# Kernel tuning notes

Measured on AMD Instinct MI355X. Metric: run time of the kernel, lower is better.

Reference implementation:

```python
import jax, jax.numpy as jnp
import numpy as np

N_NODES = 50000


def gcn_conv(x, W, b, src, dst, n):
    """PyG-style GCNConv: out = D^-1/2 (A+I) D^-1/2 (x W) + b.
    src/dst: [E] int edge endpoints (messages flow src -> dst)."""
    h = x @ W  # [n, out]
    # degree with self-loops (edge weight 1)
    deg = jax.ops.segment_sum(jnp.ones_like(dst, dtype=h.dtype), dst, num_segments=n) + 1.0
    inv_sqrt = jax.lax.rsqrt(deg)  # [n]
    coef = inv_sqrt[src] * inv_sqrt[dst]  # [E]
    msg = h[src] * coef[:, None]  # [E, out]
    agg = jax.ops.segment_sum(msg, dst, num_segments=n)
    # self-loop contribution: norm = 1/deg
    agg = agg + h * (inv_sqrt * inv_sqrt)[:, None]
    return agg + b


def encoder(x, src, dst, W_a, b_a, W_b, b_b, n):
    h = jax.nn.relu(gcn_conv(x, W_a, b_a, src, dst, n))
    return jax.nn.relu(gcn_conv(h, W_b, b_b, src, dst, n))


def setup_inputs() -> dict:
    key = jax.random.key(0)
    ks = jax.random.split(key, 8)
    N, E = N_NODES, 400000
    d_in, d_hid, d_out = 512, 512, 256
    x = jax.random.normal(ks[0], (N, d_in), dtype=jnp.float32)
    edge_index = jax.random.randint(ks[1], (2, E), 0, N, dtype=jnp.int32)
    edge_index2 = jax.random.randint(ks[2], (2, E), 0, N, dtype=jnp.int32)

    def xavier(k, shape):
        lim = np.sqrt(6.0 / (shape[0] + shape[1]))
        return jax.random.uniform(k, shape, jnp.float32, -lim, lim)

    W1 = xavier(ks[3], (d_in, d_hid))
    b1 = jnp.zeros((d_hid,), jnp.float32)
    W2 = xavier(ks[4], (d_hid, d_out))
    b2 = jnp.zeros((d_out,), jnp.float32)
    W3 = xavier(ks[5], (d_out, d_hid))
    b3 = jnp.zeros((d_hid,), jnp.float32)
    W4 = xavier(ks[6], (d_hid, d_out))
    b4 = jnp.zeros((d_out,), jnp.float32)
    return {"x": x, "edge_index": edge_index, "edge_index2": edge_index2,
            "W1": W1, "b1": b1, "W2": W2, "b2": b2,
            "W3": W3, "b3": b3, "W4": W4, "b4": b4}


def reference(x, edge_index, edge_index2, W1, b1, W2, b2, W3, b3, W4, b4):
    n = x.shape[0]
    z = encoder(x, edge_index[0], edge_index[1], W1, b1, W2, b2, n)
    z_g = encoder(z, edge_index2[0], edge_index2[1], W3, b3, W4, b4, n)
    return (z, z_g)
```

## Files before the change

### kernel.cpp

```cpp
#include <hip/hip_runtime.h>

#define N_NODES 50000
#define MP 50048

typedef short short8 __attribute__((ext_vector_type(8)));
typedef float floatx4 __attribute__((ext_vector_type(4)));
typedef ushort u16x4 __attribute__((ext_vector_type(4)));
typedef ushort u16x8 __attribute__((ext_vector_type(8)));
typedef float f32x4 __attribute__((ext_vector_type(4)));

__device__ __forceinline__ float bf2f(ushort u) {
    union { unsigned int i; float f; } x; x.i = ((unsigned int)u) << 16; return x.f;
}
__device__ __forceinline__ ushort f2bf(float f) {
    union { float f; unsigned int i; } x; x.f = f;
    unsigned int r = x.i + 0x7FFFu + ((x.i >> 16) & 1u);
    return (ushort)(r >> 16);
}

__global__ __launch_bounds__(256) void deg_int_kernel(const int* __restrict__ dst,
                                                      int* __restrict__ deg, int E) {
    int i = blockIdx.x * 256 + threadIdx.x;
    if (i < E) atomicAdd(&deg[dst[i]], 1);
}
__global__ __launch_bounds__(256) void inv_from_deg(const int* __restrict__ deg,
                                                    float* __restrict__ inv, int n) {
    int i = blockIdx.x * 256 + threadIdx.x;
    if (i < n) inv[i] = rsqrtf((float)deg[i] + 1.0f);
}

__global__ __launch_bounds__(256) void scan1_kernel(const int* __restrict__ deg,
                                                    int* __restrict__ pre,
                                                    int* __restrict__ bsum, int n) {
    __shared__ int tmp[256];
    const int t = threadIdx.x;
    const int i = blockIdx.x * 256 + t;
    const int v = (i < n) ? deg[i] : 0;
    tmp[t] = v;
    __syncthreads();
#pragma unroll
    for (int d = 1; d < 256; d <<= 1) {
        int u = (t >= d) ? tmp[t - d] : 0;
        __syncthreads();
        tmp[t] += u;
        __syncthreads();
    }
    if (i < n) pre[i] = tmp[t] - v;
    if (t == 255) bsum[blockIdx.x] = tmp[255];
}
__global__ __launch_bounds__(256) void scan2_kernel(int* __restrict__ bsum, int nb,
                                                    int* __restrict__ row_ptr_n) {
    __shared__ int tmp[256];
    const int t = threadIdx.x;
    const int v = (t < nb) ? bsum[t] : 0;
    tmp[t] = v;
    __syncthreads();
#pragma unroll
    for (int d = 1; d < 256; d <<= 1) {
        int u = (t >= d) ? tmp[t - d] : 0;
        __syncthreads();
        tmp[t] += u;
        __syncthreads();
    }
    if (t < nb) bsum[t] = tmp[t] - v;
    if (t == 255) *row_ptr_n = tmp[255];
}
__global__ __launch_bounds__(256) void scan3_kernel(const int* __restrict__ pre,
                                                    const int* __restrict__ bsum,
                                                    int* __restrict__ row_ptr,
                                                    int* __restrict__ cursor, int n) {
    const int i = blockIdx.x * 256 + threadIdx.x;
    if (i < n) {
        int v = pre[i] + bsum[blockIdx.x];
        row_ptr[i] = v;
        cursor[i] = v;
    }
}
__global__ __launch_bounds__(256) void fill_adj_kernel(const int* __restrict__ src,
                                                       const int* __restrict__ dst,
                                                       const float* __restrict__ invs,
                                                       int* __restrict__ cursor,
                                                       int2* __restrict__ adjw, int E) {
    int i = blockIdx.x * 256 + threadIdx.x;
    if (i < E) {
        int s = src[i];
        int pos = atomicAdd(&cursor[dst[i]], 1);
        adjw[pos] = make_int2(s, __float_as_int(invs[s]));
    }
}

__global__ __launch_bounds__(256) void transpose_kernel(const float* __restrict__ W,
                                                        ushort* __restrict__ Wt, int K, int N) {
    int idx = blockIdx.x * 256 + threadIdx.x;
    if (idx < K * N) {
        int k = idx / N, n = idx % N;
        Wt[n * K + k] = f2bf(W[idx]);
    }
}

__global__ __launch_bounds__(512, 4) void gemm_kernel(
    const ushort* __restrict__ A, const ushort* __restrict__ Bt,
    ushort* __restrict__ C, const float* __restrict__ bias,
    int M, int K, int N, int do_relu)
{
    __shared__ __align__(16) ushort Alds[128 * 32];
    __shared__ __align__(16) ushort Blds[128 * 32];
    const int t = threadIdx.x;
    const int w = t >> 6, l = t & 63;
    const int m0 = blockIdx.y * 128;
    const int n0 = blockIdx.x * 128;
    const int wr = (w >> 2) * 64, wc = (w & 3) * 32;
    const int lhi = l >> 4, llo = l & 15;

    floatx4 acc[4][2] = {};

    const int srow = w * 16 + (l >> 2);
    const int scol = (l & 3) * 8;
    int gr = m0 + srow; gr = gr < M ? gr : M - 1;
    const ushort* gA = A + (size_t)gr * K + scol;
    const ushort* gB = Bt + (size_t)(n0 + srow) * K + scol;
    ushort* lA = Alds + srow * 32 + scol;
    ushort* lB = Blds + srow * 32 + scol;

    const int nkt = K >> 5;
    for (int kt = 0; kt < nkt; ++kt) {
        const int k0 = kt << 5;
        __builtin_amdgcn_global_load_lds(
            (const __attribute__((address_space(1))) void*)(gA + k0),
            (__attribute__((address_space(3))) void*)lA, 16, 0, 0);
        __builtin_amdgcn_global_load_lds(
            (const __attribute__((address_space(1))) void*)(gB + k0),
            (__attribute__((address_space(3))) void*)lB, 16, 0, 0);
        __syncthreads();
        short8 av[4], bv[2];
#pragma unroll
        for (int m = 0; m < 4; ++m)
            av[m] = *reinterpret_cast<const short8*>(&Alds[(wr + m * 16 + llo) * 32 + lhi * 8]);
#pragma unroll
        for (int n = 0; n < 2; ++n)
            bv[n] = *reinterpret_cast<const short8*>(&Blds[(wc + n * 16 + llo) * 32 + lhi * 8]);
#pragma unroll
        for (int m = 0; m < 4; ++m)
#pragma unroll
            for (int n = 0; n < 2; ++n)
                acc[m][n] = __builtin_amdgcn_mfma_f32_16x16x32_bf16(av[m], bv[n], acc[m][n], 0, 0, 0);
        __syncthreads();
    }

    const int lr = lhi * 4;
#pragma unroll
    for (int m = 0; m < 4; ++m) {
#pragma unroll
        for (int n = 0; n < 2; ++n) {
            int gcol = n0 + wc + n * 16 + llo;
            float badd = bias ? bias[gcol] : 0.0f;
#pragma unroll
            for (int j = 0; j < 4; ++j) {
                int grow = m0 + wr + m * 16 + lr + j;
                if (grow < M) {
                    float v = acc[m][n][j] + badd;
                    if (do_relu) v = fmaxf(v, 0.0f);
                    C[(size_t)grow * N + gcol] = f2bf(v);
                }
            }
        }
    }
}

__global__ __launch_bounds__(512, 4) void gemm_f32a_kernel(
    const float* __restrict__ A, const ushort* __restrict__ Bt,
    ushort* __restrict__ C, int M, int K, int N)
{
    __shared__ __align__(16) ushort Alds[128 * 32];
    __shared__ __align__(16) ushort Blds[128 * 32];
    const int t = threadIdx.x;
    const int w = t >> 6, l = t & 63;
    const int m0 = blockIdx.y * 128;
    const int n0 = blockIdx.x * 128;
    const int wr = (w >> 2) * 64, wc = (w & 3) * 32;
    const int lhi = l >> 4, llo = l & 15;

    floatx4 acc[4][2] = {};

    const int srow = w * 16 + (l >> 2);
    const int scol = (l & 3) * 8;
    int gr = m0 + srow; gr = gr < M ? gr : M - 1;
    const float*  gA = A + (size_t)gr * K + scol;
    const ushort* gB = Bt + (size_t)(n0 + srow) * K + scol;
    ushort* lA = Alds + srow * 32 + scol;
    ushort* lB = Blds + srow * 32 + scol;

    const int nkt = K >> 5;
    for (int kt = 0; kt < nkt; ++kt) {
        const int k0 = kt << 5;
        __builtin_amdgcn_global_load_lds(
            (const __attribute__((address_space(1))) void*)(gB + k0),
            (__attribute__((address_space(3))) void*)lB, 16, 0, 0);
        const f32x4 alo = *reinterpret_cast<const f32x4*>(gA + k0);
        const f32x4 ahi = *reinterpret_cast<const f32x4*>(gA + k0 + 4);
        u16x8 ab;
#pragma unroll
        for (int k = 0; k < 4; ++k) { ab[k] = f2bf(alo[k]); ab[k + 4] = f2bf(ahi[k]); }
        *reinterpret_cast<u16x8*>(lA) = ab;
        __syncthreads();
        short8 av[4], bv[2];
#pragma unroll
        for (int m = 0; m < 4; ++m)
            av[m] = *reinterpret_cast<const short8*>(&Alds[(wr + m * 16 + llo) * 32 + lhi * 8]);
#pragma unroll
        for (int n = 0; n < 2; ++n)
            bv[n] = *reinterpret_cast<const short8*>(&Blds[(wc + n * 16 + llo) * 32 + lhi * 8]);
#pragma unroll
        for (int m = 0; m < 4; ++m)
#pragma unroll
            for (int n = 0; n < 2; ++n)
                acc[m][n] = __builtin_amdgcn_mfma_f32_16x16x32_bf16(av[m], bv[n], acc[m][n], 0, 0, 0);
        __syncthreads();
    }

    const int lr = lhi * 4;
#pragma unroll
    for (int m = 0; m < 4; ++m) {
#pragma unroll
        for (int n = 0; n < 2; ++n) {
            int gcol = n0 + wc + n * 16 + llo;
#pragma unroll
            for (int j = 0; j < 4; ++j) {
                int grow = m0 + wr + m * 16 + lr + j;
                if (grow < M)
                    C[(size_t)grow * N + gcol] = f2bf(acc[m][n][j]);
            }
        }
    }
}

__global__ __launch_bounds__(256) void gather512_kernel(
    const int* __restrict__ row_ptr, const int2* __restrict__ adjw,
    const ushort* __restrict__ h, const float* __restrict__ invs,
    const float* __restrict__ bias, ushort* __restrict__ outB)
{
    const int wv = threadIdx.x >> 6, l = threadIdx.x & 63;
    const int node = blockIdx.x * 4 + wv;
    if (node >= N_NODES) return;
    const int c0 = l * 8;
    const int beg = row_ptr[node], end = row_ptr[node + 1];
    const float invd = invs[node];

    float a0[8] = {}, a1[8] = {}, a2[8] = {}, a3[8] = {};
    int e = beg;
    for (; e + 4 <= end; e += 4) {
        const int2 w0 = adjw[e], w1 = adjw[e+1], w2 = adjw[e+2], w3 = adjw[e+3];
        const float f0 = __int_as_float(w0.y) * invd, f1 = __int_as_float(w1.y) * invd;
        const float f2 = __int_as_float(w2.y) * invd, f3 = __int_as_float(w3.y) * invd;
        const u16x8 h0 = *reinterpret_cast<const u16x8*>(h + (unsigned)(w0.x * 512 + c0));
        const u16x8 h1 = *reinterpret_cast<const u16x8*>(h + (unsigned)(w1.x * 512 + c0));
        const u16x8 h2 = *reinterpret_cast<const u16x8*>(h + (unsigned)(w2.x * 512 + c0));
        const u16x8 h3 = *reinterpret_cast<const u16x8*>(h + (unsigned)(w3.x * 512 + c0));
#pragma unroll
        for (int k = 0; k < 8; ++k) {
            a0[k] += bf2f(h0[k]) * f0;
            a1[k] += bf2f(h1[k]) * f1;
            a2[k] += bf2f(h2[k]) * f2;
            a3[k] += bf2f(h3[k]) * f3;
        }
    }
    if (e + 2 <= end) {
        const int2 w0 = adjw[e], w1 = adjw[e+1];
        const float f0 = __int_as_float(w0.y) * invd, f1 = __int_as_float(w1.y) * invd;
        const u16x8 h0 = *reinterpret_cast<const u16x8*>(h + (unsigned)(w0.x * 512 + c0));
        const u16x8 h1 = *reinterpret_cast<const u16x8*>(h + (unsigned)(w1.x * 512 + c0));
#pragma unroll
        for (int k = 0; k < 8; ++k) {
            a0[k] += bf2f(h0[k]) * f0;
            a1[k] += bf2f(h1[k]) * f1;
        }
        e += 2;
    }
    if (e < end) {
        const int2 w0 = adjw[e];
        const float f0 = __int_as_float(w0.y) * invd;
        const u16x8 h0 = *reinterpret_cast<const u16x8*>(h + (unsigned)(w0.x * 512 + c0));
#pragma unroll
        for (int k = 0; k < 8; ++k) a0[k] += bf2f(h0[k]) * f0;
    }
    {
        const float ws = invd * invd;
        const u16x8 hs = *reinterpret_cast<const u16x8*>(h + (unsigned)(node * 512 + c0));
#pragma unroll
        for (int k = 0; k < 8; ++k)
            a0[k] = (a0[k] + a1[k]) + (a2[k] + a3[k]) + bf2f(hs[k]) * ws;
    }
    u16x8 o;
#pragma unroll
    for (int k = 0; k < 8; ++k)
        o[k] = f2bf(fmaxf(a0[k] + bias[c0 + k], 0.0f));
    *reinterpret_cast<u16x8*>(outB + (size_t)node * 512 + c0) = o;
}

template<bool RELU, bool BIAS, bool WF, bool WB>
__global__ __launch_bounds__(256) void gather_kernel(
    const int* __restrict__ row_ptr, const int2* __restrict__ adjw,
    const ushort* __restrict__ h, int ldh,
    const float* __restrict__ invs, const float* __restrict__ bias,
    float* __restrict__ outF, ushort* __restrict__ outB, int ldo)
{
    const int wv = threadIdx.x >> 6, l = threadIdx.x & 63;
    const int node = blockIdx.x * 4 + wv;
    if (node >= N_NODES) return;
    const int c0 = l * 4;
    const int beg = row_ptr[node], end = row_ptr[node + 1];
    const float invd = invs[node];

    float a0[4] = {}, a1[4] = {}, a2[4] = {}, a3[4] = {};
    int e = beg;
    for (; e + 4 <= end; e += 4) {
        const int2 w0 = adjw[e], w1 = adjw[e+1], w2 = adjw[e+2], w3 = adjw[e+3];
        const float f0 = __int_as_float(w0.y) * invd, f1 = __int_as_float(w1.y) * invd;
        const float f2 = __int_as_float(w2.y) * invd, f3 = __int_as_float(w3.y) * invd;
        const u16x4 h0 = *reinterpret_cast<const u16x4*>(h + (unsigned)(w0.x * ldh + c0));
        const u16x4 h1 = *reinterpret_cast<const u16x4*>(h + (unsigned)(w1.x * ldh + c0));
        const u16x4 h2 = *reinterpret_cast<const u16x4*>(h + (unsigned)(w2.x * ldh + c0));
        const u16x4 h3 = *reinterpret_cast<const u16x4*>(h + (unsigned)(w3.x * ldh + c0));
#pragma unroll
        for (int k = 0; k < 4; ++k) {
            a0[k] += bf2f(h0[k]) * f0;
            a1[k] += bf2f(h1[k]) * f1;
            a2[k] += bf2f(h2[k]) * f2;
            a3[k] += bf2f(h3[k]) * f3;
        }
    }
    if (e + 2 <= end) {
        const int2 w0 = adjw[e], w1 = adjw[e+1];
        const float f0 = __int_as_float(w0.y) * invd, f1 = __int_as_float(w1.y) * invd;
        const u16x4 h0 = *reinterpret_cast<const u16x4*>(h + (unsigned)(w0.x * ldh + c0));
        const u16x4 h1 = *reinterpret_cast<const u16x4*>(h + (unsigned)(w1.x * ldh + c0));
#pragma unroll
        for (int k = 0; k < 4; ++k) {
            a0[k] += bf2f(h0[k]) * f0;
            a1[k] += bf2f(h1[k]) * f1;
        }
        e += 2;
    }
    if (e < end) {
        const int2 w0 = adjw[e];
        const float f0 = __int_as_float(w0.y) * invd;
        const u16x4 h0 = *reinterpret_cast<const u16x4*>(h + (unsigned)(w0.x * ldh + c0));
#pragma unroll
        for (int k = 0; k < 4; ++k) a0[k] += bf2f(h0[k]) * f0;
    }
    {
        const float ws = invd * invd;
        const u16x4 hs = *reinterpret_cast<const u16x4*>(h + (unsigned)(node * ldh + c0));
#pragma unroll
        for (int k = 0; k < 4; ++k)
            a0[k] = (a0[k] + a1[k]) + (a2[k] + a3[k]) + bf2f(hs[k]) * ws;
    }
#pragma unroll
    for (int k = 0; k < 4; ++k) {
        float v = a0[k];
        if (BIAS) v += bias[c0 + k];
        if (RELU) v = fmaxf(v, 0.0f);
        a0[k] = v;
    }
    if (WF)
        *reinterpret_cast<f32x4*>(outF + (size_t)node * ldo + c0) = *reinterpret_cast<f32x4*>(a0);
    if (WB) {
        u16x4 o;
#pragma unroll
        for (int k = 0; k < 4; ++k) o[k] = f2bf(a0[k]);
        *reinterpret_cast<u16x4*>(outB + (size_t)node * ldo + c0) = o;
    }
}

extern "C" void kernel_launch(void* const* d_in, const int* in_sizes, int n_in,
                              void* d_out, int out_size, void* d_ws, size_t ws_size,
                              hipStream_t stream)
{
    const float* x  = (const float*)d_in[0];
    const int* ei1  = (const int*)d_in[1];
    const int* ei2  = (const int*)d_in[2];
    const float* W1 = (const float*)d_in[3];
    const float* b1 = (const float*)d_in[4];
    const float* W2 = (const float*)d_in[5];
    const float* b2 = (const float*)d_in[6];
    const float* W3 = (const float*)d_in[7];
    const float* b3 = (const float*)d_in[8];
    const float* W4 = (const float*)d_in[9];
    const float* b4 = (const float*)d_in[10];
    float* z   = (float*)d_out;
    float* z_g = z + (size_t)N_NODES * 256;

    const int E1 = in_sizes[1] / 2, E2 = in_sizes[2] / 2;
    const int* src1 = ei1;  const int* dst1 = ei1 + E1;
    const int* src2 = ei2;  const int* dst2 = ei2 + E2;

    ushort* R1 = (ushort*)z_g;

    char* ws = (char*)d_ws;
    size_t off = 0;
    auto alloc = [&](size_t bytes) { void* p = ws + off; off += (bytes + 255) & ~(size_t)255; return p; };
    ushort* R0   = (ushort*)alloc((size_t)N_NODES * 512 * 2);
    float*  inv1 = (float*) alloc((size_t)N_NODES * 4);
    float*  inv2 = (float*) alloc((size_t)N_NODES * 4);
    int*    deg1 = (int*)   alloc((size_t)N_NODES * 4);
    int*    deg2 = (int*)   alloc((size_t)N_NODES * 4);
    int*    rp1  = (int*)   alloc((size_t)(N_NODES + 1) * 4);
    int*    rp2  = (int*)   alloc((size_t)(N_NODES + 1) * 4);
    int*    cur1 = (int*)   alloc((size_t)N_NODES * 4);
    int*    cur2 = (int*)   alloc((size_t)N_NODES * 4);
    int*    pre1 = (int*)   alloc((size_t)N_NODES * 4);
    int*    pre2 = (int*)   alloc((size_t)N_NODES * 4);
    int*    bs1  = (int*)   alloc(256 * 4);
    int*    bs2  = (int*)   alloc(256 * 4);
    int2*   adjw1= (int2*)  alloc((size_t)E1 * 8);
    int2*   adjw2= (int2*)  alloc((size_t)E2 * 8);
    ushort* Wt1  = (ushort*)alloc(512 * 512 * 2);
    ushort* Wt2  = (ushort*)alloc(256 * 512 * 2);
    ushort* Wt3  = (ushort*)alloc(512 * 256 * 2);
    ushort* Wt4  = (ushort*)alloc(256 * 512 * 2);

    const dim3 blk(256);
    const dim3 gblk(512);
    const int MT = MP / 128;
    const int GB = (N_NODES + 3) / 4;
    const int NB = (N_NODES + 255) / 256;

    hipMemsetAsync(deg1, 0, (size_t)N_NODES * 4, stream);
    hipMemsetAsync(deg2, 0, (size_t)N_NODES * 4, stream);
    deg_int_kernel<<<(E1 + 255) / 256, blk, 0, stream>>>(dst1, deg1, E1);
    deg_int_kernel<<<(E2 + 255) / 256, blk, 0, stream>>>(dst2, deg2, E2);
    inv_from_deg<<<(N_NODES + 255) / 256, blk, 0, stream>>>(deg1, inv1, N_NODES);
    inv_from_deg<<<(N_NODES + 255) / 256, blk, 0, stream>>>(deg2, inv2, N_NODES);
    scan1_kernel<<<NB, blk, 0, stream>>>(deg1, pre1, bs1, N_NODES);
    scan1_kernel<<<NB, blk, 0, stream>>>(deg2, pre2, bs2, N_NODES);
    scan2_kernel<<<1, blk, 0, stream>>>(bs1, NB, rp1 + N_NODES);
    scan2_kernel<<<1, blk, 0, stream>>>(bs2, NB, rp2 + N_NODES);
    scan3_kernel<<<NB, blk, 0, stream>>>(pre1, bs1, rp1, cur1, N_NODES);
    scan3_kernel<<<NB, blk, 0, stream>>>(pre2, bs2, rp2, cur2, N_NODES);
    fill_adj_kernel<<<(E1 + 255) / 256, blk, 0, stream>>>(src1, dst1, inv1, cur1, adjw1, E1);
    fill_adj_kernel<<<(E2 + 255) / 256, blk, 0, stream>>>(src2, dst2, inv2, cur2, adjw2, E2);

    transpose_kernel<<<(512 * 512 + 255) / 256, blk, 0, stream>>>(W1, Wt1, 512, 512);
    transpose_kernel<<<(512 * 256 + 255) / 256, blk, 0, stream>>>(W2, Wt2, 512, 256);
    transpose_kernel<<<(256 * 512 + 255) / 256, blk, 0, stream>>>(W3, Wt3, 256, 512);
    transpose_kernel<<<(512 * 256 + 255) / 256, blk, 0, stream>>>(W4, Wt4, 512, 256);

    gemm_f32a_kernel<<<dim3(4, MT), gblk, 0, stream>>>(x, Wt1, R0, N_NODES, 512, 512);
    gather512_kernel<<<GB, blk, 0, stream>>>(rp1, adjw1, R0, inv1, b1, R1);

    gemm_kernel<<<dim3(2, MT), gblk, 0, stream>>>(R1, Wt2, R0, nullptr, N_NODES, 512, 256, 0);
    gather_kernel<true, true, true, true><<<GB, blk, 0, stream>>>(
        rp1, adjw1, R0, 256, inv1, b2, z, R1, 256);

    gather_kernel<false, false, false, true><<<GB, blk, 0, stream>>>(
        rp2, adjw2, R1, 256, inv2, nullptr, nullptr, R0, 256);
    gemm_kernel<<<dim3(4, MT), gblk, 0, stream>>>(R0, Wt3, R1, b3, N_NODES, 256, 512, 1);

    gemm_kernel<<<dim3(2, MT), gblk, 0, stream>>>(R1, Wt4, R0, nullptr, N_NODES, 512, 256, 0);
    gather_kernel<true, true, true, false><<<GB, blk, 0, stream>>>(
        rp2, adjw2, R0, 256, inv2, b4, z_g, nullptr, 256);
}
```

Before: 471.0 us.

## Merge per-graph preprocessing launches and pre-convert x to bf16

```diff
diff --git a/kernel.cpp b/kernel.cpp
--- a/kernel.cpp
+++ b/kernel.cpp
@@ -18,21 +18,24 @@
     return (ushort)(r >> 16);
 }
 
-__global__ __launch_bounds__(256) void deg_int_kernel(const int* __restrict__ dst,
-                                                      int* __restrict__ deg, int E) {
+__global__ __launch_bounds__(256) void deg_both_kernel(const int* __restrict__ dst1, int E1,
+                                                       const int* __restrict__ dst2, int E2,
+                                                       int* __restrict__ deg ) {
     int i = blockIdx.x * 256 + threadIdx.x;
-    if (i < E) atomicAdd(&deg[dst[i]], 1);
-}
-__global__ __launch_bounds__(256) void inv_from_deg(const int* __restrict__ deg,
-                                                    float* __restrict__ inv, int n) {
+    if (i < E1) atomicAdd(&deg[dst1[i]], 1);
+    else if (i - E1 < E2) atomicAdd(&deg[N_NODES + dst2[i - E1]], 1);
+}
+__global__ __launch_bounds__(256) void inv_both_kernel(const int* __restrict__ deg,
+                                                       float* __restrict__ inv ) {
     int i = blockIdx.x * 256 + threadIdx.x;
-    if (i < n) inv[i] = rsqrtf((float)deg[i] + 1.0f);
-}
-
+    if (i < 2 * N_NODES) inv[i] = rsqrtf((float)deg[i] + 1.0f);
+}
 __global__ __launch_bounds__(256) void scan1_kernel(const int* __restrict__ deg,
                                                     int* __restrict__ pre,
                                                     int* __restrict__ bsum, int n) {
     __shared__ int tmp[256];
+    const int set = blockIdx.y;
+    deg += set * n; pre += set * n; bsum += set * 256;
     const int t = threadIdx.x;
     const int i = blockIdx.x * 256 + t;
     const int v = (i < n) ? deg[i] : 0;
@@ -48,9 +51,9 @@
     if (i < n) pre[i] = tmp[t] - v;
     if (t == 255) bsum[blockIdx.x] = tmp[255];
 }
-__global__ __launch_bounds__(256) void scan2_kernel(int* __restrict__ bsum, int nb,
-                                                    int* __restrict__ row_ptr_n) {
+__global__ __launch_bounds__(256) void scan2_kernel(int* __restrict__ bsum, int nb) {
     __shared__ int tmp[256];
+    bsum += blockIdx.x * 256;
     const int t = threadIdx.x;
     const int v = (t < nb) ? bsum[t] : 0;
     tmp[t] = v;
@@ -63,38 +66,65 @@
         __syncthreads();
     }
     if (t < nb) bsum[t] = tmp[t] - v;
-    if (t == 255) *row_ptr_n = tmp[255];
 }
 __global__ __launch_bounds__(256) void scan3_kernel(const int* __restrict__ pre,
                                                     const int* __restrict__ bsum,
-                                                    int* __restrict__ row_ptr,
-                                                    int* __restrict__ cursor, int n) {
+                                                    int* __restrict__ rp1, int* __restrict__ cur1,
+                                                    int* __restrict__ rp2, int* __restrict__ cur2,
+                                                    int n) {
+    const int set = blockIdx.y;
+    int* rp  = set ? rp2 : rp1;
+    int* cur = set ? cur2 : cur1;
     const int i = blockIdx.x * 256 + threadIdx.x;
     if (i < n) {
-        int v = pre[i] + bsum[blockIdx.x];
-        row_ptr[i] = v;
-        cursor[i] = v;
-    }
-}
-__global__ __launch_bounds__(256) void fill_adj_kernel(const int* __restrict__ src,
-                                                       const int* __restrict__ dst,
-                                                       const float* __restrict__ invs,
-                                                       int* __restrict__ cursor,
-                                                       int2* __restrict__ adjw, int E) {
+        int v = pre[set * n + i] + bsum[set * 256 + blockIdx.x];
+        rp[i] = v;
+        cur[i] = v;
+    }
+}
+__global__ __launch_bounds__(256) void fill_both_kernel(
+    const int* __restrict__ src1, const int* __restrict__ dst1, int E1,
+    const int* __restrict__ src2, const int* __restrict__ dst2, int E2,
+    const float* __restrict__ inv ,
+    int* __restrict__ cur1, int* __restrict__ cur2,
+    int2* __restrict__ adjw1, int2* __restrict__ adjw2) {
     int i = blockIdx.x * 256 + threadIdx.x;
-    if (i < E) {
-        int s = src[i];
-        int pos = atomicAdd(&cursor[dst[i]], 1);
-        adjw[pos] = make_int2(s, __float_as_int(invs[s]));
-    }
-}
-
-__global__ __launch_bounds__(256) void transpose_kernel(const float* __restrict__ W,
-                                                        ushort* __restrict__ Wt, int K, int N) {
+    if (i < E1) {
+        int s = src1[i];
+        int pos = atomicAdd(&cur1[dst1[i]], 1);
+        adjw1[pos] = make_int2(s, __float_as_int(inv[s]));
+    } else if (i - E1 < E2) {
+        int j = i - E1;
+        int s = src2[j];
+        int pos = atomicAdd(&cur2[dst2[j]], 1);
+        adjw2[pos] = make_int2(s, __float_as_int(inv[N_NODES + s]));
+    }
+}
+
+__global__ __launch_bounds__(256) void transpose4_kernel(
+    const float* __restrict__ W1, ushort* __restrict__ Wt1,
+    const float* __restrict__ W2, ushort* __restrict__ Wt2,
+    const float* __restrict__ W3, ushort* __restrict__ Wt3,
+    const float* __restrict__ W4, ushort* __restrict__ Wt4) {
     int idx = blockIdx.x * 256 + threadIdx.x;
-    if (idx < K * N) {
-        int k = idx / N, n = idx % N;
-        Wt[n * K + k] = f2bf(W[idx]);
+    const float* W; ushort* Wt; int K, N;
+    if (idx < 262144)      { W = W1; Wt = Wt1; K = 512; N = 512; }
+    else if (idx < 393216) { W = W2; Wt = Wt2; K = 512; N = 256; idx -= 262144; }
+    else if (idx < 524288) { W = W3; Wt = Wt3; K = 256; N = 512; idx -= 393216; }
+    else                   { W = W4; Wt = Wt4; K = 512; N = 256; idx -= 524288; }
+    int k = idx / N, n = idx % N;
+    Wt[n * K + k] = f2bf(W[idx]);
+}
+
+__global__ __launch_bounds__(256) void f2b_kernel(const float* __restrict__ in,
+                                                  ushort* __restrict__ out, int n4) {
+    int i = blockIdx.x * 256 + threadIdx.x;
+    if (i < n4) {
+        const f32x4 v = *reinterpret_cast<const f32x4*>(in + i * 4);
+        u16x4 o;
+#pragma unroll
+        for (int k = 0; k < 4; ++k) o[k] = f2bf(v[k]);
+        *reinterpret_cast<u16x4*>(out + i * 4) = o;
     }
 }
 
@@ -162,73 +192,6 @@
                     if (do_relu) v = fmaxf(v, 0.0f);
                     C[(size_t)grow * N + gcol] = f2bf(v);
                 }
-            }
-        }
-    }
-}
-
-__global__ __launch_bounds__(512, 4) void gemm_f32a_kernel(
-    const float* __restrict__ A, const ushort* __restrict__ Bt,
-    ushort* __restrict__ C, int M, int K, int N)
-{
-    __shared__ __align__(16) ushort Alds[128 * 32];
-    __shared__ __align__(16) ushort Blds[128 * 32];
-    const int t = threadIdx.x;
-    const int w = t >> 6, l = t & 63;
-    const int m0 = blockIdx.y * 128;
-    const int n0 = blockIdx.x * 128;
-    const int wr = (w >> 2) * 64, wc = (w & 3) * 32;
-    const int lhi = l >> 4, llo = l & 15;
-
-    floatx4 acc[4][2] = {};
-
-    const int srow = w * 16 + (l >> 2);
-    const int scol = (l & 3) * 8;
-    int gr = m0 + srow; gr = gr < M ? gr : M - 1;
-    const float*  gA = A + (size_t)gr * K + scol;
-    const ushort* gB = Bt + (size_t)(n0 + srow) * K + scol;
-    ushort* lA = Alds + srow * 32 + scol;
-    ushort* lB = Blds + srow * 32 + scol;
-
-    const int nkt = K >> 5;
-    for (int kt = 0; kt < nkt; ++kt) {
-        const int k0 = kt << 5;
-        __builtin_amdgcn_global_load_lds(
-            (const __attribute__((address_space(1))) void*)(gB + k0),
-            (__attribute__((address_space(3))) void*)lB, 16, 0, 0);
-        const f32x4 alo = *reinterpret_cast<const f32x4*>(gA + k0);
-        const f32x4 ahi = *reinterpret_cast<const f32x4*>(gA + k0 + 4);
-        u16x8 ab;
-#pragma unroll
-        for (int k = 0; k < 4; ++k) { ab[k] = f2bf(alo[k]); ab[k + 4] = f2bf(ahi[k]); }
-        *reinterpret_cast<u16x8*>(lA) = ab;
-        __syncthreads();
-        short8 av[4], bv[2];
-#pragma unroll
-        for (int m = 0; m < 4; ++m)
-            av[m] = *reinterpret_cast<const short8*>(&Alds[(wr + m * 16 + llo) * 32 + lhi * 8]);
-#pragma unroll
-        for (int n = 0; n < 2; ++n)
-            bv[n] = *reinterpret_cast<const short8*>(&Blds[(wc + n * 16 + llo) * 32 + lhi * 8]);
-#pragma unroll
-        for (int m = 0; m < 4; ++m)
-#pragma unroll
-            for (int n = 0; n < 2; ++n)
-                acc[m][n] = __builtin_amdgcn_mfma_f32_16x16x32_bf16(av[m], bv[n], acc[m][n], 0, 0, 0);
-        __syncthreads();
-    }
-
-    const int lr = lhi * 4;
-#pragma unroll
-    for (int m = 0; m < 4; ++m) {
-#pragma unroll
-        for (int n = 0; n < 2; ++n) {
-            int gcol = n0 + wc + n * 16 + llo;
-#pragma unroll
-            for (int j = 0; j < 4; ++j) {
-                int grow = m0 + wr + m * 16 + lr + j;
-                if (grow < M)
-                    C[(size_t)grow * N + gcol] = f2bf(acc[m][n][j]);
             }
         }
     }
@@ -394,30 +357,29 @@
     const int* src1 = ei1;  const int* dst1 = ei1 + E1;
     const int* src2 = ei2;  const int* dst2 = ei2 + E2;
 
+    ushort* Xb = (ushort*)z;
     ushort* R1 = (ushort*)z_g;
 
     char* ws = (char*)d_ws;
     size_t off = 0;
     auto alloc = [&](size_t bytes) { void* p = ws + off; off += (bytes + 255) & ~(size_t)255; return p; };
     ushort* R0   = (ushort*)alloc((size_t)N_NODES * 512 * 2);
-    float*  inv1 = (float*) alloc((size_t)N_NODES * 4);
-    float*  inv2 = (float*) alloc((size_t)N_NODES * 4);
-    int*    deg1 = (int*)   alloc((size_t)N_NODES * 4);
-    int*    deg2 = (int*)   alloc((size_t)N_NODES * 4);
+    int*    deg  = (int*)   alloc((size_t)2 * N_NODES * 4);
+    float*  inv  = (float*) alloc((size_t)2 * N_NODES * 4);
+    int*    pre  = (int*)   alloc((size_t)2 * N_NODES * 4);
+    int*    bsum = (int*)   alloc(2 * 256 * 4);
     int*    rp1  = (int*)   alloc((size_t)(N_NODES + 1) * 4);
     int*    rp2  = (int*)   alloc((size_t)(N_NODES + 1) * 4);
     int*    cur1 = (int*)   alloc((size_t)N_NODES * 4);
     int*    cur2 = (int*)   alloc((size_t)N_NODES * 4);
-    int*    pre1 = (int*)   alloc((size_t)N_NODES * 4);
-    int*    pre2 = (int*)   alloc((size_t)N_NODES * 4);
-    int*    bs1  = (int*)   alloc(256 * 4);
-    int*    bs2  = (int*)   alloc(256 * 4);
     int2*   adjw1= (int2*)  alloc((size_t)E1 * 8);
     int2*   adjw2= (int2*)  alloc((size_t)E2 * 8);
     ushort* Wt1  = (ushort*)alloc(512 * 512 * 2);
     ushort* Wt2  = (ushort*)alloc(256 * 512 * 2);
     ushort* Wt3  = (ushort*)alloc(512 * 256 * 2);
     ushort* Wt4  = (ushort*)alloc(256 * 512 * 2);
+    float*  inv1 = inv;
+    float*  inv2 = inv + N_NODES;
 
     const dim3 blk(256);
     const dim3 gblk(512);
@@ -425,27 +387,28 @@
     const int GB = (N_NODES + 3) / 4;
     const int NB = (N_NODES + 255) / 256;
 
-    hipMemsetAsync(deg1, 0, (size_t)N_NODES * 4, stream);
-    hipMemsetAsync(deg2, 0, (size_t)N_NODES * 4, stream);
-    deg_int_kernel<<<(E1 + 255) / 256, blk, 0, stream>>>(dst1, deg1, E1);
-    deg_int_kernel<<<(E2 + 255) / 256, blk, 0, stream>>>(dst2, deg2, E2);
-    inv_from_deg<<<(N_NODES + 255) / 256, blk, 0, stream>>>(deg1, inv1, N_NODES);
-    inv_from_deg<<<(N_NODES + 255) / 256, blk, 0, stream>>>(deg2, inv2, N_NODES);
-    scan1_kernel<<<NB, blk, 0, stream>>>(deg1, pre1, bs1, N_NODES);
-    scan1_kernel<<<NB, blk, 0, stream>>>(deg2, pre2, bs2, N_NODES);
-    scan2_kernel<<<1, blk, 0, stream>>>(bs1, NB, rp1 + N_NODES);
-    scan2_kernel<<<1, blk, 0, stream>>>(bs2, NB, rp2 + N_NODES);
-    scan3_kernel<<<NB, blk, 0, stream>>>(pre1, bs1, rp1, cur1, N_NODES);
-    scan3_kernel<<<NB, blk, 0, stream>>>(pre2, bs2, rp2, cur2, N_NODES);
-    fill_adj_kernel<<<(E1 + 255) / 256, blk, 0, stream>>>(src1, dst1, inv1, cur1, adjw1, E1);
-    fill_adj_kernel<<<(E2 + 255) / 256, blk, 0, stream>>>(src2, dst2, inv2, cur2, adjw2, E2);
-
-    transpose_kernel<<<(512 * 512 + 255) / 256, blk, 0, stream>>>(W1, Wt1, 512, 512);
-    transpose_kernel<<<(512 * 256 + 255) / 256, blk, 0, stream>>>(W2, Wt2, 512, 256);
-    transpose_kernel<<<(256 * 512 + 255) / 256, blk, 0, stream>>>(W3, Wt3, 256, 512);
-    transpose_kernel<<<(512 * 256 + 255) / 256, blk, 0, stream>>>(W4, Wt4, 512, 256);
-
-    gemm_f32a_kernel<<<dim3(4, MT), gblk, 0, stream>>>(x, Wt1, R0, N_NODES, 512, 512);
+    hipMemsetAsync(deg, 0, (size_t)2 * N_NODES * 4, stream);
+    deg_both_kernel<<<(E1 + E2 + 255) / 256, blk, 0, stream>>>(dst1, E1, dst2, E2, deg);
+    inv_both_kernel<<<(2 * N_NODES + 255) / 256, blk, 0, stream>>>(deg, inv);
+    scan1_kernel<<<dim3(NB, 2), blk, 0, stream>>>(deg, pre, bsum, N_NODES);
+    scan2_kernel<<<2, blk, 0, stream>>>(bsum, NB);
+    scan3_kernel<<<dim3(NB, 2), blk, 0, stream>>>(pre, bsum, rp1, cur1, rp2, cur2, N_NODES);
+    fill_both_kernel<<<(E1 + E2 + 255) / 256, blk, 0, stream>>>(
+        src1, dst1, E1, src2, dst2, E2, inv, cur1, cur2, adjw1, adjw2);
+    hipMemsetAsync(rp1 + N_NODES, 0, 4, stream);
+    hipMemsetAsync(rp2 + N_NODES, 0, 4, stream);
+
+    transpose4_kernel<<<(655360 + 255) / 256, blk, 0, stream>>>(W1, Wt1, W2, Wt2, W3, Wt3, W4, Wt4);
+    f2b_kernel<<<(N_NODES * 512 / 4 + 255) / 256, blk, 0, stream>>>(x, Xb, N_NODES * 512 / 4);
+
+    {
+        static_assert(true, "");
+    }
+    struct W { int* p; int v; };
+    extern __global__ void writeE_kernel(int* p1, int v1, int* p2, int v2);
+    writeE_kernel<<<1, 1, 0, stream>>>(rp1 + N_NODES, E1, rp2 + N_NODES, E2);
+
+    gemm_kernel<<<dim3(4, MT), gblk, 0, stream>>>(Xb, Wt1, R0, nullptr, N_NODES, 512, 512, 0);
     gather512_kernel<<<GB, blk, 0, stream>>>(rp1, adjw1, R0, inv1, b1, R1);
 
     gemm_kernel<<<dim3(2, MT), gblk, 0, stream>>>(R1, Wt2, R0, nullptr, N_NODES, 512, 256, 0);
@@ -460,3 +423,7 @@
     gather_kernel<true, true, true, false><<<GB, blk, 0, stream>>>(
         rp2, adjw2, R0, 256, inv2, b4, z_g, nullptr, 256);
 }
+
+__global__ void writeE_kernel(int* p1, int v1, int* p2, int v2) {
+    *p1 = v1; *p2 = v2;
+}
```

After: 463.2 us. Within noise of the previous version (-1.7%).
